# Optimization experiments

Measured on AMD Instinct MI355X. Metric: run time of the kernel, lower is better.

Reference implementation:

```python
import jax, jax.numpy as jnp
import numpy as np

B, N, D = 4, 512, 128
NEG = -1e9


def setup_inputs() -> dict:
    key = jax.random.key(0)
    ks = jax.random.split(key, 11)
    s = 1.0 / np.sqrt(D)
    inp = {
        "q": jax.random.normal(ks[0], (B, N, D), jnp.float32),
        "k": jax.random.normal(ks[1], (B, N, D), jnp.float32),
        "v": jax.random.normal(ks[2], (B, N, D), jnp.float32),
        "mask": jnp.ones((B, N), jnp.int32),
        # nn.Linear params: weight [out,in], bias [out]
        "Wq": jax.random.uniform(ks[3], (D, D), jnp.float32, -s, s),
        "bq": jax.random.uniform(ks[4], (D,), jnp.float32, -s, s),
        "Wk": jax.random.uniform(ks[5], (D, D), jnp.float32, -s, s),
        "bk": jax.random.uniform(ks[6], (D,), jnp.float32, -s, s),
        "Wv": jax.random.uniform(ks[7], (D, D), jnp.float32, -s, s),
        "bv": jax.random.uniform(ks[8], (D,), jnp.float32, -s, s),
        "Wo": jax.random.uniform(ks[9], (D, D), jnp.float32, -s, s),
        "bo": jax.random.uniform(ks[10], (D,), jnp.float32, -s, s),
    }
    return inp


def reference(q, k, v, mask, Wq, bq, Wk, bk, Wv, bv, Wo, bo):
    # linear projections (torch Linear: x @ W.T + b)
    qp = jnp.einsum('bnd,ed->bne', q, Wq) + bq
    kp = jnp.einsum('bnd,ed->bne', k, Wk) + bk
    vp = jnp.einsum('bnd,ed->bne', v, Wv) + bv
    # outer-product attention: scores [b, n, m, d]
    scores = jnp.einsum('bnd,bmd->bnmd', qp, kp)
    # mask [b, n] -> [b, n, 1, 1], fill masked positions with -1e9
    scores = jnp.where(mask[:, :, None, None] == 0, NEG, scores)
    # per-channel softmax over m (axis=2); dropout is a no-op at inference
    scores = jax.nn.softmax(scores, axis=2)
    out = jnp.einsum('bnmd,bmd->bnd', scores, vp)
    return jnp.einsum('bnd,ed->bne', out, Wo) + bo
```

## Files before the change

kernel.cpp:

```cpp
#include <hip/hip_runtime.h>

#define BB 4
#define NN 512
#define DD 128

static constexpr float LOG2E = 1.4426950408889634f;
#define EXP2F(x) __builtin_amdgcn_exp2f(x)

__global__ __launch_bounds__(256) void proj_kernel(
    const float* __restrict__ q, const float* __restrict__ k,
    const float* __restrict__ v, const int* __restrict__ mask,
    const float* __restrict__ Wq, const float* __restrict__ bq,
    const float* __restrict__ Wk, const float* __restrict__ bk,
    const float* __restrict__ Wv, const float* __restrict__ bv,
    float* __restrict__ qpT, float* __restrict__ kpT, float* __restrict__ vpT)
{
    __shared__ float4 sW[32 * 129];

    const int tid = threadIdx.x;
    const int t   = blockIdx.y;
    const float4* W4 = (const float4*)((t == 0) ? Wq : (t == 1) ? Wk : Wv);

    #pragma unroll
    for (int p = 0; p < 16; ++p) {
        const int f = p * 256 + tid;
        sW[(f & 31) * 129 + (f >> 5)] = W4[f];
    }
    __syncthreads();

    const int e   = tid & 127;
    const int sub = tid >> 7;
    const int r0  = blockIdx.x * 16 + sub * 8;
    const float* x    = (t == 0) ? q   : (t == 1) ? k   : v;
    const float* bias = (t == 0) ? bq  : (t == 1) ? bk  : bv;
    float*       outp = (t == 0) ? qpT : (t == 1) ? kpT : vpT;

    float acc[8] = {0.f, 0.f, 0.f, 0.f, 0.f, 0.f, 0.f, 0.f};
    #pragma unroll 4
    for (int j4 = 0; j4 < 32; ++j4) {
        const float4 w = sW[j4 * 129 + e];
        #pragma unroll
        for (int r = 0; r < 8; ++r) {
            const float4 xr = ((const float4*)(x + (r0 + r) * DD))[j4];
            acc[r] = fmaf(xr.x, w.x, fmaf(xr.y, w.y,
                     fmaf(xr.z, w.z, fmaf(xr.w, w.w, acc[r]))));
        }
    }

    const float be = bias[e];
    const int b = r0 >> 9;
    #pragma unroll
    for (int r = 0; r < 8; ++r) {
        const int g = r0 + r;
        const int n = g & (NN - 1);
        float val = acc[r] + be;
        if (t == 0) val = (mask[g] != 0) ? val * LOG2E : 0.f;
        outp[(b * DD + e) * NN + n] = val;
    }
}

__global__ __launch_bounds__(512) void attn_kernel(
    const float* __restrict__ qpT, const float* __restrict__ kpT,
    const float* __restrict__ vpT, float* __restrict__ att)
{
    __shared__ float sk[NN];
    __shared__ float sv[NN];
    __shared__ float pn[8][NN];
    __shared__ float pd[8][NN];

    const int bd  = blockIdx.x;
    const int b   = bd >> 7;
    const int d   = bd & (DD - 1);
    const int tid = threadIdx.x;
    const int h   = tid >> 6;
    const int i   = tid & 63;

    sk[tid] = kpT[bd * NN + tid];
    sv[tid] = vpT[bd * NN + tid];

    float qv[8];
    #pragma unroll
    for (int j = 0; j < 8; ++j)
        qv[j] = qpT[bd * NN + i + j * 64];
    __syncthreads();

    const float4* kc = (const float4*)sk;
    const float4* vc = (const float4*)sv;

    float na[8], da[8];
    #pragma unroll
    for (int j = 0; j < 8; ++j) { na[j] = 0.f; da[j] = 0.f; }

    const int m4lo = h * 16;
    #pragma unroll 2
    for (int m4 = m4lo; m4 < m4lo + 16; ++m4) {
        const float4 k4 = kc[m4];
        const float4 v4 = vc[m4];
        #pragma unroll
        for (int j = 0; j < 8; ++j) {
            const float p0 = EXP2F(qv[j] * k4.x);
            const float p1 = EXP2F(qv[j] * k4.y);
            const float p2 = EXP2F(qv[j] * k4.z);
            const float p3 = EXP2F(qv[j] * k4.w);
            na[j] = fmaf(p0, v4.x, na[j]);
            na[j] = fmaf(p1, v4.y, na[j]);
            na[j] = fmaf(p2, v4.z, na[j]);
            na[j] = fmaf(p3, v4.w, na[j]);
            da[j] += (p0 + p1) + (p2 + p3);
        }
    }

    #pragma unroll
    for (int j = 0; j < 8; ++j) {
        pn[h][i + j * 64] = na[j];
        pd[h][i + j * 64] = da[j];
    }
    __syncthreads();

    float num = 0.f, den = 0.f;
    #pragma unroll
    for (int hh = 0; hh < 8; ++hh) {
        num += pn[hh][tid];
        den += pd[hh][tid];
    }
    att[(b * NN + tid) * DD + d] = num / den;
}

__global__ __launch_bounds__(256) void outproj_kernel(
    const float* __restrict__ att, const float* __restrict__ Wo,
    const float* __restrict__ bo, float* __restrict__ out)
{
    __shared__ float4 sW[32 * 129];

    const int tid = threadIdx.x;
    const float4* Wo4 = (const float4*)Wo;
    #pragma unroll
    for (int p = 0; p < 16; ++p) {
        const int f = p * 256 + tid;
        sW[(f & 31) * 129 + (f >> 5)] = Wo4[f];
    }
    __syncthreads();

    const int e   = tid & 127;
    const int sub = tid >> 7;
    const int g0  = blockIdx.x * 4 + sub * 2;

    const float4* x0 = (const float4*)(att + g0 * DD);
    const float4* x1 = (const float4*)(att + (g0 + 1) * DD);

    float a0 = 0.f, a1 = 0.f;
    #pragma unroll 4
    for (int j4 = 0; j4 < 32; ++j4) {
        const float4 w  = sW[j4 * 129 + e];
        const float4 r0 = x0[j4];
        const float4 r1 = x1[j4];
        a0 = fmaf(r0.x, w.x, fmaf(r0.y, w.y, fmaf(r0.z, w.z, fmaf(r0.w, w.w, a0))));
        a1 = fmaf(r1.x, w.x, fmaf(r1.y, w.y, fmaf(r1.z, w.z, fmaf(r1.w, w.w, a1))));
    }

    const float boe = bo[e];
    out[(g0    ) * DD + e] = a0 + boe;
    out[(g0 + 1) * DD + e] = a1 + boe;
}

extern "C" void kernel_launch(void* const* d_in, const int* in_sizes, int n_in,
                              void* d_out, int out_size, void* d_ws, size_t ws_size,
                              hipStream_t stream)
{
    const float* q    = (const float*)d_in[0];
    const float* k    = (const float*)d_in[1];
    const float* v    = (const float*)d_in[2];
    const int*   mask = (const int*)  d_in[3];
    const float* Wq   = (const float*)d_in[4];
    const float* bq   = (const float*)d_in[5];
    const float* Wk   = (const float*)d_in[6];
    const float* bk   = (const float*)d_in[7];
    const float* Wv   = (const float*)d_in[8];
    const float* bv   = (const float*)d_in[9];
    const float* Wo   = (const float*)d_in[10];
    const float* bo   = (const float*)d_in[11];
    float* out = (float*)d_out;

    float* ws  = (float*)d_ws;
    float* qpT = ws;
    float* kpT = ws + 1 * BB * DD * NN;
    float* vpT = ws + 2 * BB * DD * NN;
    float* att = ws + 3 * BB * DD * NN;

    dim3 pgrid(BB * NN / 16, 3);
    proj_kernel<<<pgrid, 256, 0, stream>>>(q, k, v, mask, Wq, bq, Wk, bk,
                                           Wv, bv, qpT, kpT, vpT);

    attn_kernel<<<BB * DD, 512, 0, stream>>>(qpT, kpT, vpT, att);

    outproj_kernel<<<BB * NN / 4, 256, 0, stream>>>(att, Wo, bo, out);
}
```

Measured before the change: 120.9 us.

## Use packed float2 math in attention, transpose attention output, vectorize projection stores

The attention inner loop now uses two-wide float vectors so the multiplies and FMAs can map to packed fp32 instructions, while exp2 stays scalar. The attention output is stored channel-major (attT), which makes the attention kernel's stores contiguous. In exchange, the output projection now reads strided scalars from the transposed buffer. The projection kernel writes its 8 outputs as two float4 stores instead of eight scalar stores. The main bottleneck, the exp2 count, is unchanged, and the out-projection reads become less coalesced.

```diff
diff --git a/kernel.cpp b/kernel.cpp
--- a/kernel.cpp
+++ b/kernel.cpp
@@ -6,6 +6,8 @@
 
 static constexpr float LOG2E = 1.4426950408889634f;
 #define EXP2F(x) __builtin_amdgcn_exp2f(x)
+
+typedef float v2f __attribute__((ext_vector_type(2)));
 
 __global__ __launch_bounds__(256) void proj_kernel(
     const float* __restrict__ q, const float* __restrict__ k,
@@ -49,19 +51,22 @@
 
     const float be = bias[e];
     const int b = r0 >> 9;
+    const int n0 = r0 & (NN - 1);
+    float o[8];
     #pragma unroll
     for (int r = 0; r < 8; ++r) {
-        const int g = r0 + r;
-        const int n = g & (NN - 1);
         float val = acc[r] + be;
-        if (t == 0) val = (mask[g] != 0) ? val * LOG2E : 0.f;
-        outp[(b * DD + e) * NN + n] = val;
-    }
+        if (t == 0) val = (mask[r0 + r] != 0) ? val * LOG2E : 0.f;
+        o[r] = val;
+    }
+    float4* dst = (float4*)(outp + (b * DD + e) * NN + n0);
+    dst[0] = make_float4(o[0], o[1], o[2], o[3]);
+    dst[1] = make_float4(o[4], o[5], o[6], o[7]);
 }
 
 __global__ __launch_bounds__(512) void attn_kernel(
     const float* __restrict__ qpT, const float* __restrict__ kpT,
-    const float* __restrict__ vpT, float* __restrict__ att)
+    const float* __restrict__ vpT, float* __restrict__ attT)
 {
     __shared__ float sk[NN];
     __shared__ float sv[NN];
@@ -69,8 +74,6 @@
     __shared__ float pd[8][NN];
 
     const int bd  = blockIdx.x;
-    const int b   = bd >> 7;
-    const int d   = bd & (DD - 1);
     const int tid = threadIdx.x;
     const int h   = tid >> 6;
     const int i   = tid & 63;
@@ -78,42 +81,44 @@
     sk[tid] = kpT[bd * NN + tid];
     sv[tid] = vpT[bd * NN + tid];
 
-    float qv[8];
-    #pragma unroll
-    for (int j = 0; j < 8; ++j)
-        qv[j] = qpT[bd * NN + i + j * 64];
+    v2f qv2[8];
+    #pragma unroll
+    for (int j = 0; j < 8; ++j) {
+        const float qv = qpT[bd * NN + i + j * 64];
+        qv2[j] = (v2f){qv, qv};
+    }
     __syncthreads();
 
     const float4* kc = (const float4*)sk;
     const float4* vc = (const float4*)sv;
 
-    float na[8], da[8];
-    #pragma unroll
-    for (int j = 0; j < 8; ++j) { na[j] = 0.f; da[j] = 0.f; }
+    v2f na[8], da[8];
+    #pragma unroll
+    for (int j = 0; j < 8; ++j) { na[j] = (v2f){0.f, 0.f}; da[j] = (v2f){0.f, 0.f}; }
 
     const int m4lo = h * 16;
     #pragma unroll 2
     for (int m4 = m4lo; m4 < m4lo + 16; ++m4) {
         const float4 k4 = kc[m4];
         const float4 v4 = vc[m4];
+        const v2f kxy = (v2f){k4.x, k4.y}, kzw = (v2f){k4.z, k4.w};
+        const v2f vxy = (v2f){v4.x, v4.y}, vzw = (v2f){v4.z, v4.w};
         #pragma unroll
         for (int j = 0; j < 8; ++j) {
-            const float p0 = EXP2F(qv[j] * k4.x);
-            const float p1 = EXP2F(qv[j] * k4.y);
-            const float p2 = EXP2F(qv[j] * k4.z);
-            const float p3 = EXP2F(qv[j] * k4.w);
-            na[j] = fmaf(p0, v4.x, na[j]);
-            na[j] = fmaf(p1, v4.y, na[j]);
-            na[j] = fmaf(p2, v4.z, na[j]);
-            na[j] = fmaf(p3, v4.w, na[j]);
-            da[j] += (p0 + p1) + (p2 + p3);
+            const v2f a01 = qv2[j] * kxy;
+            const v2f a23 = qv2[j] * kzw;
+            const v2f p01 = (v2f){EXP2F(a01.x), EXP2F(a01.y)};
+            const v2f p23 = (v2f){EXP2F(a23.x), EXP2F(a23.y)};
+            na[j] = na[j] + p01 * vxy;
+            na[j] = na[j] + p23 * vzw;
+            da[j] = da[j] + (p01 + p23);
         }
     }
 
     #pragma unroll
     for (int j = 0; j < 8; ++j) {
-        pn[h][i + j * 64] = na[j];
-        pd[h][i + j * 64] = da[j];
+        pn[h][i + j * 64] = na[j].x + na[j].y;
+        pd[h][i + j * 64] = da[j].x + da[j].y;
     }
     __syncthreads();
 
@@ -123,11 +128,11 @@
         num += pn[hh][tid];
         den += pd[hh][tid];
     }
-    att[(b * NN + tid) * DD + d] = num / den;
+    attT[bd * NN + tid] = num / den;
 }
 
 __global__ __launch_bounds__(256) void outproj_kernel(
-    const float* __restrict__ att, const float* __restrict__ Wo,
+    const float* __restrict__ attT, const float* __restrict__ Wo,
     const float* __restrict__ bo, float* __restrict__ out)
 {
     __shared__ float4 sW[32 * 129];
@@ -144,18 +149,23 @@
     const int e   = tid & 127;
     const int sub = tid >> 7;
     const int g0  = blockIdx.x * 4 + sub * 2;
-
-    const float4* x0 = (const float4*)(att + g0 * DD);
-    const float4* x1 = (const float4*)(att + (g0 + 1) * DD);
+    const int b   = g0 >> 9;
+    const int n0  = g0 & (NN - 1);
+    const float* ac = attT + (b * DD) * NN;
 
     float a0 = 0.f, a1 = 0.f;
     #pragma unroll 4
     for (int j4 = 0; j4 < 32; ++j4) {
-        const float4 w  = sW[j4 * 129 + e];
-        const float4 r0 = x0[j4];
-        const float4 r1 = x1[j4];
-        a0 = fmaf(r0.x, w.x, fmaf(r0.y, w.y, fmaf(r0.z, w.z, fmaf(r0.w, w.w, a0))));
-        a1 = fmaf(r1.x, w.x, fmaf(r1.y, w.y, fmaf(r1.z, w.z, fmaf(r1.w, w.w, a1))));
+        const float4 w = sW[j4 * 129 + e];
+        #pragma unroll
+        for (int c = 0; c < 4; ++c) {
+            const int d = j4 * 4 + c;
+            const float x0 = ac[d * NN + n0];
+            const float x1 = ac[d * NN + n0 + 1];
+            const float wc = (c == 0) ? w.x : (c == 1) ? w.y : (c == 2) ? w.z : w.w;
+            a0 = fmaf(x0, wc, a0);
+            a1 = fmaf(x1, wc, a1);
+        }
     }
 
     const float boe = bo[e];
@@ -181,17 +191,17 @@
     const float* bo   = (const float*)d_in[11];
     float* out = (float*)d_out;
 
-    float* ws  = (float*)d_ws;
-    float* qpT = ws;
-    float* kpT = ws + 1 * BB * DD * NN;
-    float* vpT = ws + 2 * BB * DD * NN;
-    float* att = ws + 3 * BB * DD * NN;
+    float* ws   = (float*)d_ws;
+    float* qpT  = ws;
+    float* kpT  = ws + 1 * BB * DD * NN;
+    float* vpT  = ws + 2 * BB * DD * NN;
+    float* attT = ws + 3 * BB * DD * NN;
 
     dim3 pgrid(BB * NN / 16, 3);
     proj_kernel<<<pgrid, 256, 0, stream>>>(q, k, v, mask, Wq, bq, Wk, bk,
                                            Wv, bv, qpT, kpT, vpT);
 
-    attn_kernel<<<BB * DD, 512, 0, stream>>>(qpT, kpT, vpT, att);
-
-    outproj_kernel<<<BB * NN / 4, 256, 0, stream>>>(att, Wo, bo, out);
-}
+    attn_kernel<<<BB * DD, 512, 0, stream>>>(qpT, kpT, vpT, attT);
+
+    outproj_kernel<<<BB * NN / 4, 256, 0, stream>>>(attT, Wo, bo, out);
+}
```

Result: no change. 120.2 us (-0.5%).

## Split attention queries across blocks, halve weight tiles, store attention transposed

Applied to the files above, without the earlier changes.

The attention kernel gets a second grid dimension that splits the queries into two halves. This doubles the block count and halves per-thread registers and partial-sum shared memory, with launch bounds raised for occupancy. The projection and output kernels load weights in two half-sized shared tiles and process fewer rows per block to increase grid size, and the projection writes its outputs with float4 stores. Attention output is now written transposed so its stores are coalesced, but the output projection then reads it with strided scalar loads. Keys and values are reloaded by twice as many blocks and weights are reloaded by more blocks.

```diff
diff --git a/kernel.cpp b/kernel.cpp
--- a/kernel.cpp
+++ b/kernel.cpp
@@ -15,62 +15,68 @@
     const float* __restrict__ Wv, const float* __restrict__ bv,
     float* __restrict__ qpT, float* __restrict__ kpT, float* __restrict__ vpT)
 {
-    __shared__ float4 sW[32 * 129];
+    __shared__ float4 sW[16 * 129];
 
     const int tid = threadIdx.x;
     const int t   = blockIdx.y;
     const float4* W4 = (const float4*)((t == 0) ? Wq : (t == 1) ? Wk : Wv);
 
-    #pragma unroll
-    for (int p = 0; p < 16; ++p) {
-        const int f = p * 256 + tid;
-        sW[(f & 31) * 129 + (f >> 5)] = W4[f];
-    }
-    __syncthreads();
-
     const int e   = tid & 127;
-    const int sub = tid >> 7;
-    const int r0  = blockIdx.x * 16 + sub * 8;
+    const int sub = __builtin_amdgcn_readfirstlane(tid >> 7);
+    const int r0  = blockIdx.x * 8 + sub * 4;
     const float* x    = (t == 0) ? q   : (t == 1) ? k   : v;
     const float* bias = (t == 0) ? bq  : (t == 1) ? bk  : bv;
     float*       outp = (t == 0) ? qpT : (t == 1) ? kpT : vpT;
 
-    float acc[8] = {0.f, 0.f, 0.f, 0.f, 0.f, 0.f, 0.f, 0.f};
-    #pragma unroll 4
-    for (int j4 = 0; j4 < 32; ++j4) {
-        const float4 w = sW[j4 * 129 + e];
-        #pragma unroll
-        for (int r = 0; r < 8; ++r) {
-            const float4 xr = ((const float4*)(x + (r0 + r) * DD))[j4];
-            acc[r] = fmaf(xr.x, w.x, fmaf(xr.y, w.y,
-                     fmaf(xr.z, w.z, fmaf(xr.w, w.w, acc[r]))));
-        }
+    float acc[4] = {0.f, 0.f, 0.f, 0.f};
+
+    #pragma unroll
+    for (int half = 0; half < 2; ++half) {
+        #pragma unroll
+        for (int p = 0; p < 8; ++p) {
+            const int f = p * 256 + tid;
+            sW[(f & 15) * 129 + (f >> 4)] = W4[(f >> 4) * 32 + half * 16 + (f & 15)];
+        }
+        __syncthreads();
+
+        #pragma unroll 4
+        for (int c = 0; c < 16; ++c) {
+            const int j4 = half * 16 + c;
+            const float4 w = sW[c * 129 + e];
+            #pragma unroll
+            for (int r = 0; r < 4; ++r) {
+                const float4 xr = ((const float4*)(x + (r0 + r) * DD))[j4];
+                acc[r] = fmaf(xr.x, w.x, fmaf(xr.y, w.y,
+                         fmaf(xr.z, w.z, fmaf(xr.w, w.w, acc[r]))));
+            }
+        }
+        __syncthreads();
     }
 
     const float be = bias[e];
-    const int b = r0 >> 9;
-    #pragma unroll
-    for (int r = 0; r < 8; ++r) {
-        const int g = r0 + r;
-        const int n = g & (NN - 1);
+    const int b  = r0 >> 9;
+    const int n0 = r0 & (NN - 1);
+    float o[4];
+    #pragma unroll
+    for (int r = 0; r < 4; ++r) {
         float val = acc[r] + be;
-        if (t == 0) val = (mask[g] != 0) ? val * LOG2E : 0.f;
-        outp[(b * DD + e) * NN + n] = val;
-    }
-}
-
-__global__ __launch_bounds__(512) void attn_kernel(
+        if (t == 0) val = (mask[r0 + r] != 0) ? val * LOG2E : 0.f;
+        o[r] = val;
+    }
+    *(float4*)(outp + (b * DD + e) * NN + n0) = make_float4(o[0], o[1], o[2], o[3]);
+}
+
+__global__ __launch_bounds__(512, 8) void attn_kernel(
     const float* __restrict__ qpT, const float* __restrict__ kpT,
-    const float* __restrict__ vpT, float* __restrict__ att)
+    const float* __restrict__ vpT, float* __restrict__ attT)
 {
     __shared__ float sk[NN];
     __shared__ float sv[NN];
-    __shared__ float pn[8][NN];
-    __shared__ float pd[8][NN];
+    __shared__ float pn[8][256];
+    __shared__ float pd[8][256];
 
     const int bd  = blockIdx.x;
-    const int b   = bd >> 7;
-    const int d   = bd & (DD - 1);
+    const int qh  = blockIdx.y;
     const int tid = threadIdx.x;
     const int h   = tid >> 6;
     const int i   = tid & 63;
@@ -78,18 +84,17 @@
     sk[tid] = kpT[bd * NN + tid];
     sv[tid] = vpT[bd * NN + tid];
 
-    float qv[8];
-    #pragma unroll
-    for (int j = 0; j < 8; ++j)
-        qv[j] = qpT[bd * NN + i + j * 64];
+    float qv[4];
+    #pragma unroll
+    for (int j = 0; j < 4; ++j)
+        qv[j] = qpT[bd * NN + qh * 256 + i + j * 64];
     __syncthreads();
 
     const float4* kc = (const float4*)sk;
     const float4* vc = (const float4*)sv;
 
-    float na[8], da[8];
-    #pragma unroll
-    for (int j = 0; j < 8; ++j) { na[j] = 0.f; da[j] = 0.f; }
+    float na[4] = {0.f, 0.f, 0.f, 0.f};
+    float da[4] = {0.f, 0.f, 0.f, 0.f};
 
     const int m4lo = h * 16;
     #pragma unroll 2
@@ -97,7 +102,7 @@
         const float4 k4 = kc[m4];
         const float4 v4 = vc[m4];
         #pragma unroll
-        for (int j = 0; j < 8; ++j) {
+        for (int j = 0; j < 4; ++j) {
             const float p0 = EXP2F(qv[j] * k4.x);
             const float p1 = EXP2F(qv[j] * k4.y);
             const float p2 = EXP2F(qv[j] * k4.z);
@@ -111,56 +116,66 @@
     }
 
     #pragma unroll
-    for (int j = 0; j < 8; ++j) {
+    for (int j = 0; j < 4; ++j) {
         pn[h][i + j * 64] = na[j];
         pd[h][i + j * 64] = da[j];
     }
     __syncthreads();
 
-    float num = 0.f, den = 0.f;
-    #pragma unroll
-    for (int hh = 0; hh < 8; ++hh) {
-        num += pn[hh][tid];
-        den += pd[hh][tid];
-    }
-    att[(b * NN + tid) * DD + d] = num / den;
+    if (tid < 256) {
+        float num = 0.f, den = 0.f;
+        #pragma unroll
+        for (int hh = 0; hh < 8; ++hh) {
+            num += pn[hh][tid];
+            den += pd[hh][tid];
+        }
+        attT[bd * NN + qh * 256 + tid] = num / den;
+    }
 }
 
 __global__ __launch_bounds__(256) void outproj_kernel(
-    const float* __restrict__ att, const float* __restrict__ Wo,
+    const float* __restrict__ attT, const float* __restrict__ Wo,
     const float* __restrict__ bo, float* __restrict__ out)
 {
-    __shared__ float4 sW[32 * 129];
+    __shared__ float4 sW[16 * 129];
 
     const int tid = threadIdx.x;
     const float4* Wo4 = (const float4*)Wo;
-    #pragma unroll
-    for (int p = 0; p < 16; ++p) {
-        const int f = p * 256 + tid;
-        sW[(f & 31) * 129 + (f >> 5)] = Wo4[f];
-    }
-    __syncthreads();
 
     const int e   = tid & 127;
-    const int sub = tid >> 7;
-    const int g0  = blockIdx.x * 4 + sub * 2;
-
-    const float4* x0 = (const float4*)(att + g0 * DD);
-    const float4* x1 = (const float4*)(att + (g0 + 1) * DD);
-
-    float a0 = 0.f, a1 = 0.f;
-    #pragma unroll 4
-    for (int j4 = 0; j4 < 32; ++j4) {
-        const float4 w  = sW[j4 * 129 + e];
-        const float4 r0 = x0[j4];
-        const float4 r1 = x1[j4];
-        a0 = fmaf(r0.x, w.x, fmaf(r0.y, w.y, fmaf(r0.z, w.z, fmaf(r0.w, w.w, a0))));
-        a1 = fmaf(r1.x, w.x, fmaf(r1.y, w.y, fmaf(r1.z, w.z, fmaf(r1.w, w.w, a1))));
-    }
-
-    const float boe = bo[e];
-    out[(g0    ) * DD + e] = a0 + boe;
-    out[(g0 + 1) * DD + e] = a1 + boe;
+    const int sub = __builtin_amdgcn_readfirstlane(tid >> 7);
+    const int g   = blockIdx.x * 2 + sub;
+    const int b   = g >> 9;
+    const int n   = g & (NN - 1);
+    const float* ac = attT + (b * DD) * NN;
+
+    float acc = 0.f;
+    #pragma unroll
+    for (int half = 0; half < 2; ++half) {
+        #pragma unroll
+        for (int p = 0; p < 8; ++p) {
+            const int f = p * 256 + tid;
+            sW[(f & 15) * 129 + (f >> 4)] = Wo4[(f >> 4) * 32 + half * 16 + (f & 15)];
+        }
+        __syncthreads();
+
+        #pragma unroll 4
+        for (int c = 0; c < 16; ++c) {
+            const int j4 = half * 16 + c;
+            const float4 w = sW[c * 129 + e];
+            #pragma unroll
+            for (int cc = 0; cc < 4; ++cc) {
+                const int d = j4 * 4 + cc;
+                const float xv = ac[d * NN + n];
+                const float wc = (cc == 0) ? w.x : (cc == 1) ? w.y
+                               : (cc == 2) ? w.z : w.w;
+                acc = fmaf(xv, wc, acc);
+            }
+        }
+        __syncthreads();
+    }
+
+    out[g * DD + e] = acc + bo[e];
 }
 
 extern "C" void kernel_launch(void* const* d_in, const int* in_sizes, int n_in,
@@ -181,17 +196,18 @@
     const float* bo   = (const float*)d_in[11];
     float* out = (float*)d_out;
 
-    float* ws  = (float*)d_ws;
-    float* qpT = ws;
-    float* kpT = ws + 1 * BB * DD * NN;
-    float* vpT = ws + 2 * BB * DD * NN;
-    float* att = ws + 3 * BB * DD * NN;
-
-    dim3 pgrid(BB * NN / 16, 3);
+    float* ws   = (float*)d_ws;
+    float* qpT  = ws;
+    float* kpT  = ws + 1 * BB * DD * NN;
+    float* vpT  = ws + 2 * BB * DD * NN;
+    float* attT = ws + 3 * BB * DD * NN;
+
+    dim3 pgrid(BB * NN / 8, 3);
     proj_kernel<<<pgrid, 256, 0, stream>>>(q, k, v, mask, Wq, bq, Wk, bk,
                                            Wv, bv, qpT, kpT, vpT);
 
-    attn_kernel<<<BB * DD, 512, 0, stream>>>(qpT, kpT, vpT, att);
-
-    outproj_kernel<<<BB * NN / 4, 256, 0, stream>>>(att, Wo, bo, out);
-}
+    dim3 agrid(BB * DD, 2);
+    attn_kernel<<<agrid, 512, 0, stream>>>(qpT, kpT, vpT, attT);
+
+    outproj_kernel<<<BB * NN / 2, 256, 0, stream>>>(attT, Wo, bo, out);
+}
```

Result: faster. 111.8 us (-7.5%).
